# Kernel optimization log

Measured on AMD Instinct MI355X. Metric: run time of the kernel, lower is better.

Reference implementation:

```python
import jax, jax.numpy as jnp
import numpy as np

# ---- module hyperparameters (match init_kwargs) ----
SPATIAL = (32, 64)          # token grid, N = 32*64 = 2048
D_MODEL = 1024
N_HEADS = 16
HEAD_DIM = D_MODEL // N_HEADS  # 64
THETA = 10000.0
XPOS_SCALE_BASE = SPATIAL[0] * 2  # 64


def _rope_tables():
    """ND rotary (xpos) tables, lucidrains-style.
    Each spatial axis gets head_dim//ndim rotary channels; frequencies are
    interleave-repeated (r=2) to pair with rotate_half. Returns cos, sin,
    xpos scale, each [N, HEAD_DIM] float32."""
    nd = len(SPATIAL)
    dpa = HEAD_DIM // nd  # dims per axis (32)
    freqs_axes, scale_axes = [], []
    for size in SPATIAL:
        inv_freq = 1.0 / (THETA ** (np.arange(0, dpa, 2, dtype=np.float64) / dpa))
        t = np.arange(size, dtype=np.float64)
        f = np.repeat(t[:, None] * inv_freq[None, :], 2, axis=-1)        # [size, dpa]
        sbase = (np.arange(0, dpa, 2, dtype=np.float64) + 0.4 * dpa) / (1.4 * dpa)
        power = (t - size // 2) / XPOS_SCALE_BASE
        sc = np.repeat(sbase[None, :] ** power[:, None], 2, axis=-1)     # [size, dpa]
        freqs_axes.append(f)
        scale_axes.append(sc)
    # broadcast each axis table over the full grid, concat along channel dim
    def grid_concat(tabs):
        parts = []
        for i, tab in enumerate(tabs):
            shp = [1] * nd + [dpa]
            shp[i] = SPATIAL[i]
            parts.append(np.broadcast_to(tab.reshape(shp), tuple(SPATIAL) + (dpa,)))
        return np.concatenate(parts, axis=-1).reshape(-1, HEAD_DIM)  # [N, HEAD_DIM]
    freqs = grid_concat(freqs_axes)
    xscale = grid_concat(scale_axes)
    return (jnp.asarray(np.cos(freqs), jnp.float32),
            jnp.asarray(np.sin(freqs), jnp.float32),
            jnp.asarray(xscale, jnp.float32))


def _rotate_half(x):
    # pairwise rotation: (x1, x2) -> (-x2, x1), interleaved layout
    x = x.reshape(*x.shape[:-1], -1, 2)
    x1, x2 = x[..., 0], x[..., 1]
    return jnp.stack((-x2, x1), axis=-1).reshape(*x.shape[:-2], -1)


def setup_inputs() -> dict:
    key = jax.random.key(0)
    ks = jax.random.split(key, 3)
    B, N = 2, SPATIAL[0] * SPATIAL[1]
    x = jax.random.normal(ks[0], (B, N, D_MODEL), dtype=jnp.float32)
    w_qkv = jax.random.normal(ks[1], (D_MODEL, 3 * D_MODEL), dtype=jnp.float32) * 0.02
    b_qkv = jnp.zeros((3 * D_MODEL,), jnp.float32)
    w_proj = jax.random.normal(ks[2], (D_MODEL, D_MODEL), dtype=jnp.float32) * 0.02
    b_proj = jnp.zeros((D_MODEL,), jnp.float32)
    return {"x": x, "w_qkv": w_qkv, "b_qkv": b_qkv, "w_proj": w_proj, "b_proj": b_proj}


def reference(x, w_qkv, b_qkv, w_proj, b_proj):
    B, N, C = x.shape
    scale = HEAD_DIM ** -0.5
    qkv = (x @ w_qkv + b_qkv).reshape(B, N, 3, N_HEADS, HEAD_DIM)
    qkv = qkv.transpose(2, 0, 3, 1, 4)  # [3, B, H, N, D]
    q, k, v = qkv[0], qkv[1], qkv[2]
    cos, sin, xs = _rope_tables()       # [N, D], broadcast over B,H
    q = (q * cos + _rotate_half(q) * sin) * xs
    k = (k * cos + _rotate_half(k) * sin) / xs
    attn = jax.nn.softmax(jnp.einsum('bhnd,bhmd->bhnm', q, k) * scale, axis=-1)
    out = jnp.einsum('bhnm,bhmd->bhnd', attn, v)
    out = out.transpose(0, 2, 1, 3).reshape(B, N, C)
    return out @ w_proj + b_proj
```

## Files before the change

kernel.cpp:

```cpp
#include <hip/hip_runtime.h>
#include <math.h>

typedef __attribute__((ext_vector_type(8))) _Float16 f16x8;
typedef __attribute__((ext_vector_type(4))) _Float16 f16x4;
typedef __attribute__((ext_vector_type(4))) float f32x4;

#define MFMAH(a, b, c) __builtin_amdgcn_mfma_f32_16x16x32_f16((a), (b), (c), 0, 0, 0)

#define QSCALE 0.18033688011112042f
#define SOFF 4.328085122666891f


__global__ void cast_f16_kernel(const float* __restrict__ in, _Float16* __restrict__ out, int n) {
    int i = blockIdx.x * 256 + threadIdx.x;
    if (i >= n) return;
    out[i] = (_Float16)in[i];
}

__global__ void transpose_cast_f16_kernel(const float* __restrict__ in,
                                          _Float16* __restrict__ out, int C) {
    int i = blockIdx.x * 256 + threadIdx.x;
    if (i >= (C << 10)) return;
    int c = i >> 10;
    int r = i & 1023;
    out[i] = (_Float16)in[(size_t)r * C + c];
}

__global__ void rope_tables_kernel(float* __restrict__ ct, float* __restrict__ st,
                                   float* __restrict__ xt) {
    int i = blockIdx.x * 256 + threadIdx.x;
    if (i >= 2048 * 64) return;
    int n = i >> 6, d = i & 63;
    int gi = n >> 6, gj = n & 63;
    int axis = d >> 5;
    int p = (d & 31) >> 1;
    float t = axis ? (float)gj : (float)gi;
    float half = axis ? 32.0f : 16.0f;
    float inv_freq = powf(10000.0f, -(float)p * (1.0f / 16.0f));
    float fr = t * inv_freq;
    float sbase = (2.0f * p + 12.8f) / 44.8f;
    float xs = powf(sbase, (t - half) * (1.0f / 64.0f));
    ct[i] = cosf(fr);
    st[i] = sinf(fr);
    xt[i] = xs;
}

#define LDK 40

__global__ __launch_bounds__(256) void gemm_qkv_kernel(
    const _Float16* __restrict__ A_g, const _Float16* __restrict__ B_g,
    const float* __restrict__ bias, const float* __restrict__ ctab,
    const float* __restrict__ stab, const float* __restrict__ xtab,
    _Float16* __restrict__ qb, _Float16* __restrict__ kb, _Float16* __restrict__ vt) {
    __shared__ __align__(16) _Float16 Asm[128 * LDK];
    __shared__ __align__(16) _Float16 Bsm[128 * LDK];

    const int tid = threadIdx.x;
    const int lane = tid & 63, wave = tid >> 6;
    const int quad = lane >> 4, l16 = lane & 15;
    const int wm = wave >> 1, wn = wave & 1;
    const int m0 = blockIdx.x * 128, n0 = blockIdx.y * 128;

    f32x4 zero = {0.f, 0.f, 0.f, 0.f};
    f32x4 acc[4][4];
#pragma unroll
    for (int i = 0; i < 4; ++i)
#pragma unroll
        for (int j = 0; j < 4; ++j) acc[i][j] = zero;

    const int r0 = tid >> 2, o0 = (tid & 3) << 3;
    const int r1 = (tid + 256) >> 2, o1 = ((tid + 256) & 3) << 3;
    const size_t ab = (size_t)m0 * 1024;
    const size_t bb = (size_t)n0 * 1024;

    f16x8 pa0 = *(const f16x8*)&A_g[ab + (size_t)r0 * 1024 + o0];
    f16x8 pa1 = *(const f16x8*)&A_g[ab + (size_t)r1 * 1024 + o1];
    f16x8 pb0 = *(const f16x8*)&B_g[bb + (size_t)r0 * 1024 + o0];
    f16x8 pb1 = *(const f16x8*)&B_g[bb + (size_t)r1 * 1024 + o1];

    for (int k0 = 0; k0 < 1024; k0 += 32) {
        __syncthreads();
        *(f16x8*)&Asm[r0 * LDK + o0] = pa0;
        *(f16x8*)&Asm[r1 * LDK + o1] = pa1;
        *(f16x8*)&Bsm[r0 * LDK + o0] = pb0;
        *(f16x8*)&Bsm[r1 * LDK + o1] = pb1;
        __syncthreads();

        if (k0 + 32 < 1024) {
            const int kn = k0 + 32;
            pa0 = *(const f16x8*)&A_g[ab + kn + (size_t)r0 * 1024 + o0];
            pa1 = *(const f16x8*)&A_g[ab + kn + (size_t)r1 * 1024 + o1];
            pb0 = *(const f16x8*)&B_g[bb + kn + (size_t)r0 * 1024 + o0];
            pb1 = *(const f16x8*)&B_g[bb + kn + (size_t)r1 * 1024 + o1];
        }

        f16x8 af[4], bf[4];
#pragma unroll
        for (int i = 0; i < 4; ++i) {
            af[i] = *(const f16x8*)&Asm[(wm * 64 + i * 16 + l16) * LDK + quad * 8];
            bf[i] = *(const f16x8*)&Bsm[(wn * 64 + i * 16 + l16) * LDK + quad * 8];
        }
#pragma unroll
        for (int i = 0; i < 4; ++i)
#pragma unroll
            for (int j = 0; j < 4; ++j) acc[i][j] = MFMAH(af[i], bf[j], acc[i][j]);
    }

    float bj[4];
#pragma unroll
    for (int j = 0; j < 4; ++j) bj[j] = bias[n0 + wn * 64 + j * 16 + l16];

    if (n0 < 2048) {
#pragma unroll
        for (int i = 0; i < 4; ++i) {
#pragma unroll
            for (int r = 0; r < 4; ++r) {
                const int row = m0 + wm * 64 + i * 16 + quad * 4 + r;
                const int b = row >> 11, nrow = row & 2047;
#pragma unroll
                for (int j = 0; j < 4; ++j) {
                    const int col = n0 + wn * 64 + j * 16 + l16;
                    float v = acc[i][j][r] + bj[j];
                    float partner = __shfl_xor(v, 1);
                    const int hh = (col >> 6) & 15;
                    const int d = col & 63;
                    const size_t o = ((size_t)(b * 16 + hh) * 2048 + nrow) * 64 + d;
                    float rh = (d & 1) ? partner : -partner;
                    const int ti = nrow * 64 + d;
                    float rv = v * ctab[ti] + rh * stab[ti];
                    float xs = xtab[ti];
                    if (col < 1024)
                        qb[o] = (_Float16)(rv * xs * QSCALE);
                    else
                        kb[o] = (_Float16)(rv / xs);
                }
            }
        }
    } else {
#pragma unroll
        for (int i = 0; i < 4; ++i) {
            const int row = m0 + wm * 64 + i * 16 + quad * 4;
            const int b = row >> 11, nrow = row & 2047;
#pragma unroll
            for (int j = 0; j < 4; ++j) {
                const int col = n0 + wn * 64 + j * 16 + l16;
                const int hh = (col >> 6) & 15;
                const int d = col & 63;
                f16x4 pv4;
#pragma unroll
                for (int r = 0; r < 4; ++r) pv4[r] = (_Float16)(acc[i][j][r] + bj[j]);
                *(f16x4*)&vt[((size_t)(b * 16 + hh) * 64 + d) * 2048 + nrow] = pv4;
            }
        }
    }
}

__global__ __launch_bounds__(256) void gemm_proj_kernel(
    const _Float16* __restrict__ A_g, const _Float16* __restrict__ B_g,
    const float* __restrict__ bias, float* __restrict__ out) {
    __shared__ __align__(16) _Float16 Asm[128 * LDK];
    __shared__ __align__(16) _Float16 Bsm[128 * LDK];

    const int tid = threadIdx.x;
    const int lane = tid & 63, wave = tid >> 6;
    const int quad = lane >> 4, l16 = lane & 15;
    const int wm = wave >> 1, wn = wave & 1;
    const int m0 = blockIdx.x * 128, n0 = blockIdx.y * 128;

    f32x4 zero = {0.f, 0.f, 0.f, 0.f};
    f32x4 acc[4][4];
#pragma unroll
    for (int i = 0; i < 4; ++i)
#pragma unroll
        for (int j = 0; j < 4; ++j) acc[i][j] = zero;

    const int r0 = tid >> 2, o0 = (tid & 3) << 3;
    const int r1 = (tid + 256) >> 2, o1 = ((tid + 256) & 3) << 3;
    const size_t ab = (size_t)m0 * 1024;
    const size_t bb = (size_t)n0 * 1024;

    f16x8 pa0 = *(const f16x8*)&A_g[ab + (size_t)r0 * 1024 + o0];
    f16x8 pa1 = *(const f16x8*)&A_g[ab + (size_t)r1 * 1024 + o1];
    f16x8 pb0 = *(const f16x8*)&B_g[bb + (size_t)r0 * 1024 + o0];
    f16x8 pb1 = *(const f16x8*)&B_g[bb + (size_t)r1 * 1024 + o1];

    for (int k0 = 0; k0 < 1024; k0 += 32) {
        __syncthreads();
        *(f16x8*)&Asm[r0 * LDK + o0] = pa0;
        *(f16x8*)&Asm[r1 * LDK + o1] = pa1;
        *(f16x8*)&Bsm[r0 * LDK + o0] = pb0;
        *(f16x8*)&Bsm[r1 * LDK + o1] = pb1;
        __syncthreads();

        if (k0 + 32 < 1024) {
            const int kn = k0 + 32;
            pa0 = *(const f16x8*)&A_g[ab + kn + (size_t)r0 * 1024 + o0];
            pa1 = *(const f16x8*)&A_g[ab + kn + (size_t)r1 * 1024 + o1];
            pb0 = *(const f16x8*)&B_g[bb + kn + (size_t)r0 * 1024 + o0];
            pb1 = *(const f16x8*)&B_g[bb + kn + (size_t)r1 * 1024 + o1];
        }

        f16x8 af[4], bf[4];
#pragma unroll
        for (int i = 0; i < 4; ++i) {
            af[i] = *(const f16x8*)&Asm[(wm * 64 + i * 16 + l16) * LDK + quad * 8];
            bf[i] = *(const f16x8*)&Bsm[(wn * 64 + i * 16 + l16) * LDK + quad * 8];
        }
#pragma unroll
        for (int i = 0; i < 4; ++i)
#pragma unroll
            for (int j = 0; j < 4; ++j) acc[i][j] = MFMAH(af[i], bf[j], acc[i][j]);
    }

    float bj[4];
#pragma unroll
    for (int j = 0; j < 4; ++j) bj[j] = bias[n0 + wn * 64 + j * 16 + l16];
#pragma unroll
    for (int i = 0; i < 4; ++i)
#pragma unroll
        for (int r = 0; r < 4; ++r) {
            const int row = m0 + wm * 64 + i * 16 + quad * 4 + r;
#pragma unroll
            for (int j = 0; j < 4; ++j) {
                const int col = n0 + wn * 64 + j * 16 + l16;
                out[(size_t)row * 1024 + col] = acc[i][j][r] + bj[j];
            }
        }
}

#define KLD 72
#define PLD 72

__global__ __launch_bounds__(256) void attn_kernel(
    const _Float16* __restrict__ qb, const _Float16* __restrict__ kb,
    const _Float16* __restrict__ vt, _Float16* __restrict__ ao) {
    __shared__ __align__(16) _Float16 Ksm[64 * KLD];
    __shared__ __align__(16) _Float16 Vsm[64 * KLD];
    __shared__ __align__(16) _Float16 Psm[4 * 32 * PLD];

    const int tid = threadIdx.x;
    const int lane = tid & 63, wave = tid >> 6;
    const int quad = lane >> 4, l16 = lane & 15;
    const int qt = blockIdx.x & 15, bh = blockIdx.x >> 4;
    const size_t base = (size_t)bh * 2048 * 64;
    const int qrow0 = qt * 128 + wave * 32;

    f16x8 qf[2][2];
#pragma unroll
    for (int rg = 0; rg < 2; ++rg) {
        qf[rg][0] = *(const f16x8*)&qb[base + (size_t)(qrow0 + rg * 16 + l16) * 64 + quad * 8];
        qf[rg][1] = *(const f16x8*)&qb[base + (size_t)(qrow0 + rg * 16 + l16) * 64 + 32 + quad * 8];
    }

    f32x4 zero = {0.f, 0.f, 0.f, 0.f};
    f32x4 moff = {-SOFF, -SOFF, -SOFF, -SOFF};
    f32x4 o[2][4];
    float lsum[2] = {0.f, 0.f};
#pragma unroll
    for (int rg = 0; rg < 2; ++rg)
#pragma unroll
        for (int dc = 0; dc < 4; ++dc) o[rg][dc] = zero;

    const int kr0 = tid >> 3, ko0 = (tid & 7) << 3;
    const int kr1 = (tid + 256) >> 3, ko1 = ((tid + 256) & 7) << 3;
    f16x8 pk[2], pv[2];

    pk[0] = *(const f16x8*)&kb[base + (size_t)kr0 * 64 + ko0];
    pk[1] = *(const f16x8*)&kb[base + (size_t)kr1 * 64 + ko1];
    pv[0] = *(const f16x8*)&vt[((size_t)bh * 64 + kr0) * 2048 + ko0];
    pv[1] = *(const f16x8*)&vt[((size_t)bh * 64 + kr1) * 2048 + ko1];

    _Float16* Pw = &Psm[wave * 32 * PLD];

    for (int it = 0; it < 32; ++it) {
        __syncthreads();
        *(f16x8*)&Ksm[kr0 * KLD + ko0] = pk[0];
        *(f16x8*)&Ksm[kr1 * KLD + ko1] = pk[1];
        *(f16x8*)&Vsm[kr0 * KLD + ko0] = pv[0];
        *(f16x8*)&Vsm[kr1 * KLD + ko1] = pv[1];
        __syncthreads();

        if (it + 1 < 32) {
            const int kt = (it + 1) * 64;
            pk[0] = *(const f16x8*)&kb[base + (size_t)(kt + kr0) * 64 + ko0];
            pk[1] = *(const f16x8*)&kb[base + (size_t)(kt + kr1) * 64 + ko1];
            pv[0] = *(const f16x8*)&vt[((size_t)bh * 64 + kr0) * 2048 + kt + ko0];
            pv[1] = *(const f16x8*)&vt[((size_t)bh * 64 + kr1) * 2048 + kt + ko1];
        }

        f32x4 s[2][4];
#pragma unroll
        for (int kg = 0; kg < 4; ++kg) {
            f16x8 kf0 = *(const f16x8*)&Ksm[(kg * 16 + l16) * KLD + quad * 8];
            f16x8 kf1 = *(const f16x8*)&Ksm[(kg * 16 + l16) * KLD + 32 + quad * 8];
            s[0][kg] = MFMAH(kf0, qf[0][0], moff);
            s[0][kg] = MFMAH(kf1, qf[0][1], s[0][kg]);
            s[1][kg] = MFMAH(kf0, qf[1][0], moff);
            s[1][kg] = MFMAH(kf1, qf[1][1], s[1][kg]);
        }

#pragma unroll
        for (int rg = 0; rg < 2; ++rg)
#pragma unroll
            for (int kg = 0; kg < 4; ++kg) {
                float p0 = __builtin_amdgcn_exp2f(s[rg][kg][0]);
                float p1 = __builtin_amdgcn_exp2f(s[rg][kg][1]);
                float p2 = __builtin_amdgcn_exp2f(s[rg][kg][2]);
                float p3 = __builtin_amdgcn_exp2f(s[rg][kg][3]);
                lsum[rg] += (p0 + p1) + (p2 + p3);
                f16x4 ph = {(_Float16)p0, (_Float16)p1, (_Float16)p2, (_Float16)p3};
                *(f16x4*)&Pw[(rg * 16 + l16) * PLD + kg * 16 + quad * 4] = ph;
            }

        f16x8 pf[2][2];
#pragma unroll
        for (int rg = 0; rg < 2; ++rg) {
            pf[rg][0] = *(const f16x8*)&Pw[(rg * 16 + l16) * PLD + quad * 8];
            pf[rg][1] = *(const f16x8*)&Pw[(rg * 16 + l16) * PLD + 32 + quad * 8];
        }
#pragma unroll
        for (int dc = 0; dc < 4; ++dc) {
            f16x8 vf0 = *(const f16x8*)&Vsm[(dc * 16 + l16) * KLD + quad * 8];
            f16x8 vf1 = *(const f16x8*)&Vsm[(dc * 16 + l16) * KLD + 32 + quad * 8];
#pragma unroll
            for (int rg = 0; rg < 2; ++rg) {
                o[rg][dc] = MFMAH(pf[rg][0], vf0, o[rg][dc]);
                o[rg][dc] = MFMAH(pf[rg][1], vf1, o[rg][dc]);
            }
        }
    }

    float linv[2][4];
#pragma unroll
    for (int rg = 0; rg < 2; ++rg) {
        float v = lsum[rg];
        v += __shfl_xor(v, 16);
        v += __shfl_xor(v, 32);
        v = 1.0f / v;
#pragma unroll
        for (int r = 0; r < 4; ++r) linv[rg][r] = __shfl(v, quad * 4 + r);
    }

    const int b = bh >> 4, hh = bh & 15;
#pragma unroll
    for (int rg = 0; rg < 2; ++rg)
#pragma unroll
        for (int dc = 0; dc < 4; ++dc)
#pragma unroll
            for (int r = 0; r < 4; ++r) {
                float v = o[rg][dc][r] * linv[rg][r];
                const int qrow = qrow0 + rg * 16 + quad * 4 + r;
                const size_t oi = ((size_t)(b * 2048 + qrow)) * 1024 + hh * 64 + dc * 16 + l16;
                ao[oi] = (_Float16)v;
            }
}

extern "C" void kernel_launch(void* const* d_in, const int* in_sizes, int n_in,
                              void* d_out, int out_size, void* d_ws, size_t ws_size,
                              hipStream_t stream) {
    const float* x = (const float*)d_in[0];
    const float* w_qkv = (const float*)d_in[1];
    const float* b_qkv = (const float*)d_in[2];
    const float* w_proj = (const float*)d_in[3];
    const float* b_proj = (const float*)d_in[4];
    float* out = (float*)d_out;

    char* ws = (char*)d_ws;
    size_t off = 0;
    auto take = [&](size_t bytes) { char* p = ws + off; off += bytes; return p; };
    _Float16* xbuf   = (_Float16*)take(8388608);
    _Float16* wqkvT  = (_Float16*)take(6291456);
    _Float16* wprojT = (_Float16*)take(2097152);
    _Float16* qbuf   = (_Float16*)take(8388608);
    _Float16* kbuf   = (_Float16*)take(8388608);
    _Float16* vtbuf  = (_Float16*)take(8388608);
    float* ctab      = (float*)take(524288);
    float* stab      = (float*)take(524288);
    float* xtab      = (float*)take(524288);
    _Float16* ao = xbuf;

    cast_f16_kernel<<<16384, 256, 0, stream>>>(x, xbuf, 4194304);
    transpose_cast_f16_kernel<<<12288, 256, 0, stream>>>(w_qkv, wqkvT, 3072);
    transpose_cast_f16_kernel<<<4096, 256, 0, stream>>>(w_proj, wprojT, 1024);
    rope_tables_kernel<<<512, 256, 0, stream>>>(ctab, stab, xtab);
    gemm_qkv_kernel<<<dim3(32, 24), 256, 0, stream>>>(xbuf, wqkvT, b_qkv,
                                                      ctab, stab, xtab, qbuf, kbuf, vtbuf);
    attn_kernel<<<512, 256, 0, stream>>>(qbuf, kbuf, vtbuf, ao);
    gemm_proj_kernel<<<dim3(32, 8), 256, 0, stream>>>(ao, wprojT, b_proj, out);
}
```

Measured before the change: 231.5 us.

## Merge prep kernels, shrink proj GEMM N-tile, reorder attention block mapping

Four preprocessing kernels (x cast, two weight transpose-casts, rope tables) are merged into one launch that branches on block index. This removes launch gaps between them. The projection GEMM tile shrinks from 128x128 to 128x64, doubling the grid from 256 to 512 blocks to fill more CUs, at the cost of more A re-reads. The attention kernel's block-to-(bh, q-tile) mapping is swapped so consecutive blocks work on different heads, and the load index math is simplified.

```diff
diff --git a/kernel.cpp b/kernel.cpp
--- a/kernel.cpp
+++ b/kernel.cpp
@@ -10,39 +10,39 @@
 #define QSCALE 0.18033688011112042f
 #define SOFF 4.328085122666891f
 
-
-__global__ void cast_f16_kernel(const float* __restrict__ in, _Float16* __restrict__ out, int n) {
-    int i = blockIdx.x * 256 + threadIdx.x;
-    if (i >= n) return;
-    out[i] = (_Float16)in[i];
-}
-
-__global__ void transpose_cast_f16_kernel(const float* __restrict__ in,
-                                          _Float16* __restrict__ out, int C) {
-    int i = blockIdx.x * 256 + threadIdx.x;
-    if (i >= (C << 10)) return;
-    int c = i >> 10;
-    int r = i & 1023;
-    out[i] = (_Float16)in[(size_t)r * C + c];
-}
-
-__global__ void rope_tables_kernel(float* __restrict__ ct, float* __restrict__ st,
-                                   float* __restrict__ xt) {
-    int i = blockIdx.x * 256 + threadIdx.x;
-    if (i >= 2048 * 64) return;
-    int n = i >> 6, d = i & 63;
-    int gi = n >> 6, gj = n & 63;
-    int axis = d >> 5;
-    int p = (d & 31) >> 1;
-    float t = axis ? (float)gj : (float)gi;
-    float half = axis ? 32.0f : 16.0f;
-    float inv_freq = powf(10000.0f, -(float)p * (1.0f / 16.0f));
-    float fr = t * inv_freq;
-    float sbase = (2.0f * p + 12.8f) / 44.8f;
-    float xs = powf(sbase, (t - half) * (1.0f / 64.0f));
-    ct[i] = cosf(fr);
-    st[i] = sinf(fr);
-    xt[i] = xs;
+__global__ void prep_kernel(const float* __restrict__ x, const float* __restrict__ w_qkv,
+                            const float* __restrict__ w_proj, _Float16* __restrict__ xb,
+                            _Float16* __restrict__ wq, _Float16* __restrict__ wp,
+                            float* __restrict__ ct, float* __restrict__ st,
+                            float* __restrict__ xt) {
+    const int b = blockIdx.x, tid = threadIdx.x;
+    if (b < 16384) {
+        int i = b * 256 + tid;
+        xb[i] = (_Float16)x[i];
+    } else if (b < 28672) {
+        int i = (b - 16384) * 256 + tid;
+        int c = i >> 10, r = i & 1023;
+        wq[i] = (_Float16)w_qkv[(size_t)r * 3072 + c];
+    } else if (b < 32768) {
+        int i = (b - 28672) * 256 + tid;
+        int c = i >> 10, r = i & 1023;
+        wp[i] = (_Float16)w_proj[(size_t)r * 1024 + c];
+    } else {
+        int i = (b - 32768) * 256 + tid;
+        int n = i >> 6, d = i & 63;
+        int gi = n >> 6, gj = n & 63;
+        int axis = d >> 5;
+        int p = (d & 31) >> 1;
+        float t = axis ? (float)gj : (float)gi;
+        float half = axis ? 32.0f : 16.0f;
+        float inv_freq = powf(10000.0f, -(float)p * (1.0f / 16.0f));
+        float fr = t * inv_freq;
+        float sbase = (2.0f * p + 12.8f) / 44.8f;
+        float xs = powf(sbase, (t - half) * (1.0f / 64.0f));
+        ct[i] = cosf(fr);
+        st[i] = sinf(fr);
+        xt[i] = xs;
+    }
 }
 
 #define LDK 40
@@ -69,29 +69,28 @@
         for (int j = 0; j < 4; ++j) acc[i][j] = zero;
 
     const int r0 = tid >> 2, o0 = (tid & 3) << 3;
-    const int r1 = (tid + 256) >> 2, o1 = ((tid + 256) & 3) << 3;
     const size_t ab = (size_t)m0 * 1024;
     const size_t bb = (size_t)n0 * 1024;
 
     f16x8 pa0 = *(const f16x8*)&A_g[ab + (size_t)r0 * 1024 + o0];
-    f16x8 pa1 = *(const f16x8*)&A_g[ab + (size_t)r1 * 1024 + o1];
+    f16x8 pa1 = *(const f16x8*)&A_g[ab + (size_t)(r0 + 64) * 1024 + o0];
     f16x8 pb0 = *(const f16x8*)&B_g[bb + (size_t)r0 * 1024 + o0];
-    f16x8 pb1 = *(const f16x8*)&B_g[bb + (size_t)r1 * 1024 + o1];
+    f16x8 pb1 = *(const f16x8*)&B_g[bb + (size_t)(r0 + 64) * 1024 + o0];
 
     for (int k0 = 0; k0 < 1024; k0 += 32) {
         __syncthreads();
         *(f16x8*)&Asm[r0 * LDK + o0] = pa0;
-        *(f16x8*)&Asm[r1 * LDK + o1] = pa1;
+        *(f16x8*)&Asm[(r0 + 64) * LDK + o0] = pa1;
         *(f16x8*)&Bsm[r0 * LDK + o0] = pb0;
-        *(f16x8*)&Bsm[r1 * LDK + o1] = pb1;
+        *(f16x8*)&Bsm[(r0 + 64) * LDK + o0] = pb1;
         __syncthreads();
 
         if (k0 + 32 < 1024) {
             const int kn = k0 + 32;
             pa0 = *(const f16x8*)&A_g[ab + kn + (size_t)r0 * 1024 + o0];
-            pa1 = *(const f16x8*)&A_g[ab + kn + (size_t)r1 * 1024 + o1];
+            pa1 = *(const f16x8*)&A_g[ab + kn + (size_t)(r0 + 64) * 1024 + o0];
             pb0 = *(const f16x8*)&B_g[bb + kn + (size_t)r0 * 1024 + o0];
-            pb1 = *(const f16x8*)&B_g[bb + kn + (size_t)r1 * 1024 + o1];
+            pb1 = *(const f16x8*)&B_g[bb + kn + (size_t)(r0 + 64) * 1024 + o0];
         }
 
         f16x8 af[4], bf[4];
@@ -159,70 +158,67 @@
     const _Float16* __restrict__ A_g, const _Float16* __restrict__ B_g,
     const float* __restrict__ bias, float* __restrict__ out) {
     __shared__ __align__(16) _Float16 Asm[128 * LDK];
-    __shared__ __align__(16) _Float16 Bsm[128 * LDK];
+    __shared__ __align__(16) _Float16 Bsm[64 * LDK];
 
     const int tid = threadIdx.x;
     const int lane = tid & 63, wave = tid >> 6;
     const int quad = lane >> 4, l16 = lane & 15;
     const int wm = wave >> 1, wn = wave & 1;
-    const int m0 = blockIdx.x * 128, n0 = blockIdx.y * 128;
+    const int m0 = blockIdx.x * 128, n0 = blockIdx.y * 64;
 
     f32x4 zero = {0.f, 0.f, 0.f, 0.f};
-    f32x4 acc[4][4];
+    f32x4 acc[4][2];
 #pragma unroll
     for (int i = 0; i < 4; ++i)
 #pragma unroll
-        for (int j = 0; j < 4; ++j) acc[i][j] = zero;
+        for (int j = 0; j < 2; ++j) acc[i][j] = zero;
 
     const int r0 = tid >> 2, o0 = (tid & 3) << 3;
-    const int r1 = (tid + 256) >> 2, o1 = ((tid + 256) & 3) << 3;
     const size_t ab = (size_t)m0 * 1024;
     const size_t bb = (size_t)n0 * 1024;
 
     f16x8 pa0 = *(const f16x8*)&A_g[ab + (size_t)r0 * 1024 + o0];
-    f16x8 pa1 = *(const f16x8*)&A_g[ab + (size_t)r1 * 1024 + o1];
+    f16x8 pa1 = *(const f16x8*)&A_g[ab + (size_t)(r0 + 64) * 1024 + o0];
     f16x8 pb0 = *(const f16x8*)&B_g[bb + (size_t)r0 * 1024 + o0];
-    f16x8 pb1 = *(const f16x8*)&B_g[bb + (size_t)r1 * 1024 + o1];
 
     for (int k0 = 0; k0 < 1024; k0 += 32) {
         __syncthreads();
         *(f16x8*)&Asm[r0 * LDK + o0] = pa0;
-        *(f16x8*)&Asm[r1 * LDK + o1] = pa1;
+        *(f16x8*)&Asm[(r0 + 64) * LDK + o0] = pa1;
         *(f16x8*)&Bsm[r0 * LDK + o0] = pb0;
-        *(f16x8*)&Bsm[r1 * LDK + o1] = pb1;
         __syncthreads();
 
         if (k0 + 32 < 1024) {
             const int kn = k0 + 32;
             pa0 = *(const f16x8*)&A_g[ab + kn + (size_t)r0 * 1024 + o0];
-            pa1 = *(const f16x8*)&A_g[ab + kn + (size_t)r1 * 1024 + o1];
+            pa1 = *(const f16x8*)&A_g[ab + kn + (size_t)(r0 + 64) * 1024 + o0];
             pb0 = *(const f16x8*)&B_g[bb + kn + (size_t)r0 * 1024 + o0];
-            pb1 = *(const f16x8*)&B_g[bb + kn + (size_t)r1 * 1024 + o1];
-        }
-
-        f16x8 af[4], bf[4];
-#pragma unroll
-        for (int i = 0; i < 4; ++i) {
+        }
+
+        f16x8 af[4], bf[2];
+#pragma unroll
+        for (int i = 0; i < 4; ++i)
             af[i] = *(const f16x8*)&Asm[(wm * 64 + i * 16 + l16) * LDK + quad * 8];
-            bf[i] = *(const f16x8*)&Bsm[(wn * 64 + i * 16 + l16) * LDK + quad * 8];
-        }
+#pragma unroll
+        for (int j = 0; j < 2; ++j)
+            bf[j] = *(const f16x8*)&Bsm[(wn * 32 + j * 16 + l16) * LDK + quad * 8];
 #pragma unroll
         for (int i = 0; i < 4; ++i)
 #pragma unroll
-            for (int j = 0; j < 4; ++j) acc[i][j] = MFMAH(af[i], bf[j], acc[i][j]);
-    }
-
-    float bj[4];
-#pragma unroll
-    for (int j = 0; j < 4; ++j) bj[j] = bias[n0 + wn * 64 + j * 16 + l16];
+            for (int j = 0; j < 2; ++j) acc[i][j] = MFMAH(af[i], bf[j], acc[i][j]);
+    }
+
+    float bj[2];
+#pragma unroll
+    for (int j = 0; j < 2; ++j) bj[j] = bias[n0 + wn * 32 + j * 16 + l16];
 #pragma unroll
     for (int i = 0; i < 4; ++i)
 #pragma unroll
         for (int r = 0; r < 4; ++r) {
             const int row = m0 + wm * 64 + i * 16 + quad * 4 + r;
 #pragma unroll
-            for (int j = 0; j < 4; ++j) {
-                const int col = n0 + wn * 64 + j * 16 + l16;
+            for (int j = 0; j < 2; ++j) {
+                const int col = n0 + wn * 32 + j * 16 + l16;
                 out[(size_t)row * 1024 + col] = acc[i][j][r] + bj[j];
             }
         }
@@ -241,7 +237,7 @@
     const int tid = threadIdx.x;
     const int lane = tid & 63, wave = tid >> 6;
     const int quad = lane >> 4, l16 = lane & 15;
-    const int qt = blockIdx.x & 15, bh = blockIdx.x >> 4;
+    const int bh = blockIdx.x & 31, qt = blockIdx.x >> 5;
     const size_t base = (size_t)bh * 2048 * 64;
     const int qrow0 = qt * 128 + wave * 32;
 
@@ -252,8 +248,8 @@
         qf[rg][1] = *(const f16x8*)&qb[base + (size_t)(qrow0 + rg * 16 + l16) * 64 + 32 + quad * 8];
     }
 
+    f32x4 moff = {-SOFF, -SOFF, -SOFF, -SOFF};
     f32x4 zero = {0.f, 0.f, 0.f, 0.f};
-    f32x4 moff = {-SOFF, -SOFF, -SOFF, -SOFF};
     f32x4 o[2][4];
     float lsum[2] = {0.f, 0.f};
 #pragma unroll
@@ -262,30 +258,30 @@
         for (int dc = 0; dc < 4; ++dc) o[rg][dc] = zero;
 
     const int kr0 = tid >> 3, ko0 = (tid & 7) << 3;
-    const int kr1 = (tid + 256) >> 3, ko1 = ((tid + 256) & 7) << 3;
-    f16x8 pk[2], pv[2];
-
-    pk[0] = *(const f16x8*)&kb[base + (size_t)kr0 * 64 + ko0];
-    pk[1] = *(const f16x8*)&kb[base + (size_t)kr1 * 64 + ko1];
-    pv[0] = *(const f16x8*)&vt[((size_t)bh * 64 + kr0) * 2048 + ko0];
-    pv[1] = *(const f16x8*)&vt[((size_t)bh * 64 + kr1) * 2048 + ko1];
+    const int kr1 = kr0 + 32;
+    f16x8 pk0, pk1, pv0, pv1;
+
+    pk0 = *(const f16x8*)&kb[base + (size_t)kr0 * 64 + ko0];
+    pk1 = *(const f16x8*)&kb[base + (size_t)kr1 * 64 + ko0];
+    pv0 = *(const f16x8*)&vt[((size_t)bh * 64 + kr0) * 2048 + ko0];
+    pv1 = *(const f16x8*)&vt[((size_t)bh * 64 + kr1) * 2048 + ko0];
 
     _Float16* Pw = &Psm[wave * 32 * PLD];
 
     for (int it = 0; it < 32; ++it) {
         __syncthreads();
-        *(f16x8*)&Ksm[kr0 * KLD + ko0] = pk[0];
-        *(f16x8*)&Ksm[kr1 * KLD + ko1] = pk[1];
-        *(f16x8*)&Vsm[kr0 * KLD + ko0] = pv[0];
-        *(f16x8*)&Vsm[kr1 * KLD + ko1] = pv[1];
+        *(f16x8*)&Ksm[kr0 * KLD + ko0] = pk0;
+        *(f16x8*)&Ksm[kr1 * KLD + ko0] = pk1;
+        *(f16x8*)&Vsm[kr0 * KLD + ko0] = pv0;
+        *(f16x8*)&Vsm[kr1 * KLD + ko0] = pv1;
         __syncthreads();
 
         if (it + 1 < 32) {
             const int kt = (it + 1) * 64;
-            pk[0] = *(const f16x8*)&kb[base + (size_t)(kt + kr0) * 64 + ko0];
-            pk[1] = *(const f16x8*)&kb[base + (size_t)(kt + kr1) * 64 + ko1];
-            pv[0] = *(const f16x8*)&vt[((size_t)bh * 64 + kr0) * 2048 + kt + ko0];
-            pv[1] = *(const f16x8*)&vt[((size_t)bh * 64 + kr1) * 2048 + kt + ko1];
+            pk0 = *(const f16x8*)&kb[base + (size_t)(kt + kr0) * 64 + ko0];
+            pk1 = *(const f16x8*)&kb[base + (size_t)(kt + kr1) * 64 + ko0];
+            pv0 = *(const f16x8*)&vt[((size_t)bh * 64 + kr0) * 2048 + kt + ko0];
+            pv1 = *(const f16x8*)&vt[((size_t)bh * 64 + kr1) * 2048 + kt + ko0];
         }
 
         f32x4 s[2][4];
@@ -379,12 +375,10 @@
     float* xtab      = (float*)take(524288);
     _Float16* ao = xbuf;
 
-    cast_f16_kernel<<<16384, 256, 0, stream>>>(x, xbuf, 4194304);
-    transpose_cast_f16_kernel<<<12288, 256, 0, stream>>>(w_qkv, wqkvT, 3072);
-    transpose_cast_f16_kernel<<<4096, 256, 0, stream>>>(w_proj, wprojT, 1024);
-    rope_tables_kernel<<<512, 256, 0, stream>>>(ctab, stab, xtab);
+    prep_kernel<<<33280, 256, 0, stream>>>(x, w_qkv, w_proj, xbuf, wqkvT, wprojT,
+                                           ctab, stab, xtab);
     gemm_qkv_kernel<<<dim3(32, 24), 256, 0, stream>>>(xbuf, wqkvT, b_qkv,
                                                       ctab, stab, xtab, qbuf, kbuf, vtbuf);
     attn_kernel<<<512, 256, 0, stream>>>(qbuf, kbuf, vtbuf, ao);
-    gemm_proj_kernel<<<dim3(32, 8), 256, 0, stream>>>(ao, wprojT, b_proj, out);
-}
+    gemm_proj_kernel<<<dim3(32, 16), 256, 0, stream>>>(ao, wprojT, b_proj, out);
+}
```

After: 222.9 us. 1.04x faster.
